# Kernel optimization log

Hardware: AMD Instinct MI355X
Metric: run time of the kernel (lower is better)

Reference implementation:

```python
import jax, jax.numpy as jnp
import numpy as np

PAD = float(-2**32 + 1)


def setup_inputs() -> dict:
    key = jax.random.key(0)
    ks = jax.random.split(key, 10)
    B, S, D = 8, 1024, 1024
    s = 0.02  # keep projections in sane range
    return {
        "Q": jax.random.normal(ks[0], (B, S, D), jnp.float32),
        "K": jax.random.normal(ks[1], (B, S, D), jnp.float32),
        "V": jax.random.normal(ks[2], (B, S, D), jnp.float32),
        "WQ": jax.random.normal(ks[3], (D, D), jnp.float32) * s,
        "bQ": jnp.zeros((D,), jnp.float32),
        "WK": jax.random.normal(ks[4], (D, D), jnp.float32) * s,
        "bK": jnp.zeros((D,), jnp.float32),
        "WV": jax.random.normal(ks[5], (D, D), jnp.float32) * s,
        "bV": jnp.zeros((D,), jnp.float32),
        "WO": jax.random.normal(ks[6], (D, D), jnp.float32) * s,
        "bO": jnp.zeros((D,), jnp.float32),
        "h": 16,
    }


def reference(Q, K, V, WQ, bQ, WK, bK, WV, bV, WO, bO, h):
    B, S, D = Q.shape
    dk = D // h
    # Dense projections with relu activation (as in the Keras layer)
    Qp = jax.nn.relu(Q @ WQ + bQ)
    Kp = jax.nn.relu(K @ WK + bK)
    Vp = jax.nn.relu(V @ WV + bV)
    # tf.concat(tf.split(x, h, axis=2), axis=0): head-major stacking -> (h, B, S, dk)
    qh = Qp.reshape(B, S, h, dk).transpose(2, 0, 1, 3)
    kh = Kp.reshape(B, S, h, dk).transpose(2, 0, 1, 3)
    vh = Vp.reshape(B, S, h, dk).transpose(2, 0, 1, 3)
    # scaled dot product; NOTE: source scales by 1/sqrt(d_model), not 1/sqrt(d_k)
    scores = jnp.einsum('hbqd,hbkd->hbqk', qh, kh) / jnp.sqrt(jnp.float32(D))
    # key padding mask: zero key rows -> large negative
    kmask = jnp.sum(jnp.abs(kh), axis=-1) != 0  # (h,B,Tk)
    scores = jnp.where(kmask[:, :, None, :], scores, PAD)
    w = jax.nn.softmax(scores, axis=-1)
    # query padding mask: zero query rows -> zero weights
    qmask = jnp.sign(jnp.sum(jnp.abs(qh), axis=-1))  # (h,B,Tq), 0/1
    w = w * qmask[:, :, :, None]
    # dropout_prob = 0.0 -> identity
    out = jnp.einsum('hbqk,hbkd->hbqd', w, vh)
    # tf.concat(tf.split(dot_product, h, axis=0), axis=2) -> (B,S,h*dk)
    out = out.transpose(1, 2, 0, 3).reshape(B, S, D)
    return jax.nn.relu(out @ WO + bO)
```

## Files before the change

kernel.cpp:

```cpp
#include <hip/hip_runtime.h>
#include <hip/hip_bf16.h>
#include <cstdint>

#define DEV __device__ __forceinline__

typedef __attribute__((ext_vector_type(4))) float f32x4;
typedef __attribute__((ext_vector_type(8))) short b16x8;
typedef __attribute__((ext_vector_type(4))) unsigned short u16x4;
typedef __attribute__((ext_vector_type(8))) unsigned short u16x8;
typedef __attribute__((ext_vector_type(2))) unsigned int u32x2;

typedef __attribute__((address_space(1))) void gvoid_t;
typedef __attribute__((address_space(3))) void lvoid_t;

static constexpr int Bsz = 8, Ssz = 1024, Dsz = 1024;
static constexpr int Mrows = Bsz * Ssz;

DEV void gld16(const void* g, void* l) {
  __builtin_amdgcn_global_load_lds((gvoid_t*)(uintptr_t)g,
                                   (lvoid_t*)(unsigned)(uintptr_t)l, 16, 0, 0);
}

DEV unsigned short f2bf(float x) {
  unsigned int u = __float_as_uint(x);
  u += 0x7fffu + ((u >> 16) & 1u);
  return (unsigned short)(u >> 16);
}

DEV unsigned int cvt2(float lo, float hi) {
  __hip_bfloat162 h = __float22bfloat162_rn(make_float2(lo, hi));
  unsigned int u;
  __builtin_memcpy(&u, &h, 4);
  return u;
}

__global__ __launch_bounds__(256) void wconv_kernel(
    const float* __restrict__ WQ, const float* __restrict__ WK,
    const float* __restrict__ WV, const float* __restrict__ WO,
    unsigned short* __restrict__ Wt) {
  __shared__ float tile[64][65];
  const int w = blockIdx.z;
  const float* W = (w == 0) ? WQ : (w == 1) ? WK : (w == 2) ? WV : WO;
  const int k0 = blockIdx.x * 64, n0 = blockIdx.y * 64;
  const int t = threadIdx.x;
  {
    const int r = t >> 4;
    const int c = (t & 15) * 4;
#pragma unroll
    for (int i = 0; i < 4; ++i) {
      f32x4 v = *(const f32x4*)(W + (size_t)(k0 + i * 16 + r) * Dsz + n0 + c);
      tile[i * 16 + r][c + 0] = v[0];
      tile[i * 16 + r][c + 1] = v[1];
      tile[i * 16 + r][c + 2] = v[2];
      tile[i * 16 + r][c + 3] = v[3];
    }
  }
  __syncthreads();
  {
    const int n = t >> 2;
    const int ks = (t & 3) * 16;
    unsigned short* dst =
        Wt + (size_t)w * Dsz * Dsz + (size_t)(n0 + n) * Dsz + k0 + ks;
#pragma unroll
    for (int j = 0; j < 16; j += 4) {
      u16x4 p;
#pragma unroll
      for (int jj = 0; jj < 4; ++jj) p[jj] = f2bf(tile[ks + j + jj][n]);
      *(u16x4*)(dst + j) = p;
    }
  }
}

template <bool A_FP32, int OUT_MODE>
DEV void gemm_body(const void* __restrict__ A_,
                   const unsigned short* __restrict__ Bt,
                   const float* __restrict__ bias, void* __restrict__ C_,
                   int m0, int n0, float outscale) {
  constexpr int Kd = 1024, Nd = 1024;
  __shared__ unsigned short Asl[128 * 64] __attribute__((aligned(16)));
  __shared__ unsigned short Bsl[128 * 64] __attribute__((aligned(16)));
  const int t = threadIdx.x, lane = t & 63, wave = t >> 6;
  const int grp = lane >> 4, r16 = lane & 15;
  const int wm = wave >> 1, wn = wave & 1;
  const int swz = (r16 & 7) << 4;
  f32x4 acc[4][4] = {};
  for (int kt = 0; kt < Kd; kt += 64) {
#pragma unroll
    for (int j = 0; j < 4; ++j) {
      int chunk = (wave * 4 + j) * 64 + lane;
      int row = chunk >> 3, c = chunk & 7;
      int csw = c ^ (row & 7);
      gld16(Bt + (size_t)(n0 + row) * Kd + kt + csw * 8,
            (char*)Bsl + (wave * 4 + j) * 1024);
      if constexpr (!A_FP32) {
        gld16((const unsigned short*)A_ + (size_t)(m0 + row) * Kd + kt + csw * 8,
              (char*)Asl + (wave * 4 + j) * 1024);
      }
    }
    if constexpr (A_FP32) {
      const float* A = (const float*)A_;
#pragma unroll
      for (int it = 0; it < 4; ++it) {
        int chunk = it * 256 + t;
        int row = chunk >> 3, c = chunk & 7;
        int csw = c ^ (row & 7);
        const float* src = A + (size_t)(m0 + row) * Kd + kt + csw * 8;
        f32x4 v0 = *(const f32x4*)src;
        f32x4 v1 = *(const f32x4*)(src + 4);
        u32x2 w0, w1;
        w0[0] = cvt2(v0[0], v0[1]);
        w0[1] = cvt2(v0[2], v0[3]);
        w1[0] = cvt2(v1[0], v1[1]);
        w1[1] = cvt2(v1[2], v1[3]);
        *(u32x2*)((char*)Asl + chunk * 16) = w0;
        *(u32x2*)((char*)Asl + chunk * 16 + 8) = w1;
      }
    }
    __syncthreads();
#pragma unroll
    for (int cs = 0; cs < 2; ++cs) {
      b16x8 af[4], bfr[4];
#pragma unroll
      for (int mi = 0; mi < 4; ++mi)
        af[mi] = *(const b16x8*)((char*)Asl + (wm * 64 + mi * 16 + r16) * 128 +
                                 ((cs * 64 + grp * 16) ^ swz));
#pragma unroll
      for (int ni = 0; ni < 4; ++ni)
        bfr[ni] = *(const b16x8*)((char*)Bsl + (wn * 64 + ni * 16 + r16) * 128 +
                                  ((cs * 64 + grp * 16) ^ swz));
#pragma unroll
      for (int mi = 0; mi < 4; ++mi)
#pragma unroll
        for (int ni = 0; ni < 4; ++ni)
          acc[mi][ni] = __builtin_amdgcn_mfma_f32_16x16x32_bf16(
              af[mi], bfr[ni], acc[mi][ni], 0, 0, 0);
    }
    __syncthreads();
  }
#pragma unroll
  for (int mi = 0; mi < 4; ++mi) {
#pragma unroll
    for (int ni = 0; ni < 4; ++ni) {
      int col = n0 + wn * 64 + ni * 16 + r16;
      float bv = bias[col];
      int row0 = m0 + wm * 64 + mi * 16 + grp * 4;
      if constexpr (OUT_MODE == 2) {
        int bb = row0 >> 10, s = row0 & 1023;
        u16x4 pk;
#pragma unroll
        for (int r = 0; r < 4; ++r)
          pk[r] = f2bf(fmaxf(acc[mi][ni][r] + bv, 0.0f) * outscale);
        *(u16x4*)((unsigned short*)C_ +
                  (((size_t)(bb * 1024 + col)) << 10) + s) = pk;
      } else {
#pragma unroll
        for (int r = 0; r < 4; ++r) {
          float v = fmaxf(acc[mi][ni][r] + bv, 0.0f) * outscale;
          if constexpr (OUT_MODE == 1)
            ((unsigned short*)C_)[(size_t)(row0 + r) * Nd + col] = f2bf(v);
          else
            ((float*)C_)[(size_t)(row0 + r) * Nd + col] = v;
        }
      }
    }
  }
}

static constexpr float QSCALE = 0.03125f * 1.4426950408889634f;

__global__ __launch_bounds__(256) void proj3_kernel(
    const float* __restrict__ Q, const float* __restrict__ K,
    const float* __restrict__ V, const unsigned short* __restrict__ Wt,
    const float* __restrict__ bQ, const float* __restrict__ bK,
    const float* __restrict__ bV, unsigned short* __restrict__ Qp,
    unsigned short* __restrict__ Kp, unsigned short* __restrict__ VpT) {
  const size_t DD = (size_t)Dsz * Dsz;
  const int bid = blockIdx.x;
  const int id2 = (bid & 7) * 64 + (bid >> 3);
  const int n0 = (id2 & 7) * 128, m0 = (id2 >> 3) * 128;
  const int z = blockIdx.z;
  if (z == 0)
    gemm_body<true, 1>(Q, Wt, bQ, Qp, m0, n0, QSCALE);
  else if (z == 1)
    gemm_body<true, 1>(K, Wt + DD, bK, Kp, m0, n0, 1.0f);
  else
    gemm_body<true, 2>(V, Wt + 2 * DD, bV, VpT, m0, n0, 1.0f);
}

__global__ __launch_bounds__(256) void out_gemm_kernel(
    const unsigned short* __restrict__ AO,
    const unsigned short* __restrict__ WOt, const float* __restrict__ bO,
    float* __restrict__ Out) {
  const int bid = blockIdx.x;
  const int id2 = (bid & 7) * 64 + (bid >> 3);
  const int n0 = (id2 & 7) * 128, m0 = (id2 >> 3) * 128;
  gemm_body<false, 0>(AO, WOt, bO, Out, m0, n0, 1.0f);
}

__global__ __launch_bounds__(512, 4) void attn_kernel(
    const unsigned short* __restrict__ Qp, const unsigned short* __restrict__ Kp,
    const unsigned short* __restrict__ VpT, unsigned short* __restrict__ AO) {
  __shared__ unsigned short Ks[2][64 * 64] __attribute__((aligned(16)));
  __shared__ unsigned short Vs[2][64 * 64] __attribute__((aligned(16)));
  __shared__ unsigned short Ps[16][16 * 64] __attribute__((aligned(16)));
  const int t = threadIdx.x, lane = t & 63, wave = t >> 6;
  const int grp = lane >> 4, r16 = lane & 15;
  const int bid = blockIdx.x;
  const int id2 = (bid & 7) * 64 + (bid >> 3);
  const int q0 = (id2 & 3) * 256;
  const int bh = id2 >> 2;
  const int b = bh & 7, head = bh >> 3;

  const int srow = t >> 3, scc = t & 7;
  const int csw = scc ^ (srow & 7);
  const unsigned short* kbase = Kp + ((size_t)b * Ssz) * Dsz + head * 64;
  const unsigned short* vbase = VpT + ((size_t)b * Dsz + head * 64) * Ssz;

  const int sqA = q0 + wave * 16 + r16;
  const unsigned short* qbA = Qp + ((size_t)b * Ssz + sqA) * Dsz + head * 64;
  const unsigned short* qbB = qbA + (size_t)128 * Dsz;
  b16x8 qfA0 = *(const b16x8*)(qbA + grp * 8);
  b16x8 qfA1 = *(const b16x8*)(qbA + 32 + grp * 8);
  b16x8 qfB0 = *(const b16x8*)(qbB + grp * 8);
  b16x8 qfB1 = *(const b16x8*)(qbB + 32 + grp * 8);

  f32x4 oA[4] = {}, oB[4] = {};
  f32x4 olA = {}, olB = {};
  const f32x4 zero4 = {0.0f, 0.0f, 0.0f, 0.0f};
  const b16x8 ones = {16256, 16256, 16256, 16256,
                      16256, 16256, 16256, 16256};

  auto stage = [&](int kv0, int pb) {
    gld16(kbase + (size_t)(kv0 + srow) * Dsz + csw * 8,
          (char*)Ks[pb] + wave * 1024);
    gld16(vbase + (size_t)srow * Ssz + kv0 + csw * 8,
          (char*)Vs[pb] + wave * 1024);
  };

  stage(0, 0);
  __syncthreads();
  int cur = 0;

  for (int it = 0; it < 16; ++it) {
    if (it < 15) stage((it + 1) * 64, cur ^ 1);

    __builtin_amdgcn_s_setprio(1);
    f32x4 scA[4], scB[4];
#pragma unroll
    for (int f = 0; f < 4; ++f) {
      int k = f * 16 + r16;
      int kswz = (k & 7) << 4;
      const char* kb = (const char*)Ks[cur] + k * 128;
      b16x8 kf0 = *(const b16x8*)(kb + ((grp * 16) ^ kswz));
      b16x8 kf1 = *(const b16x8*)(kb + ((64 + grp * 16) ^ kswz));
      f32x4 sA = __builtin_amdgcn_mfma_f32_16x16x32_bf16(kf0, qfA0, zero4, 0, 0, 0);
      scA[f] = __builtin_amdgcn_mfma_f32_16x16x32_bf16(kf1, qfA1, sA, 0, 0, 0);
      f32x4 sB = __builtin_amdgcn_mfma_f32_16x16x32_bf16(kf0, qfB0, zero4, 0, 0, 0);
      scB[f] = __builtin_amdgcn_mfma_f32_16x16x32_bf16(kf1, qfB1, sB, 0, 0, 0);
    }
    __builtin_amdgcn_s_setprio(0);

    {
      int qs = (r16 & 7) << 4;
      char* prowA = (char*)Ps + (wave * 2 + 0) * 2048 + r16 * 128;
      char* prowB = (char*)Ps + (wave * 2 + 1) * 2048 + r16 * 128;
#pragma unroll
      for (int f = 0; f < 4; ++f) {
        u32x2 w;
        w[0] = cvt2(exp2f(scA[f][0]), exp2f(scA[f][1]));
        w[1] = cvt2(exp2f(scA[f][2]), exp2f(scA[f][3]));
        *(u32x2*)(prowA + ((f * 32 + grp * 8) ^ qs)) = w;
      }
#pragma unroll
      for (int f = 0; f < 4; ++f) {
        u32x2 w;
        w[0] = cvt2(exp2f(scB[f][0]), exp2f(scB[f][1]));
        w[1] = cvt2(exp2f(scB[f][2]), exp2f(scB[f][3]));
        *(u32x2*)(prowB + ((f * 32 + grp * 8) ^ qs)) = w;
      }
    }

    __builtin_amdgcn_s_setprio(1);
#pragma unroll
    for (int ks = 0; ks < 2; ++ks) {
      int pswz = (r16 & 7) << 4;
      int poff = r16 * 128 + ((ks * 64 + grp * 16) ^ pswz);
      b16x8 paA = *(const b16x8*)((char*)Ps + (wave * 2 + 0) * 2048 + poff);
      b16x8 paB = *(const b16x8*)((char*)Ps + (wave * 2 + 1) * 2048 + poff);
      olA = __builtin_amdgcn_mfma_f32_16x16x32_bf16(paA, ones, olA, 0, 0, 0);
      olB = __builtin_amdgcn_mfma_f32_16x16x32_bf16(paB, ones, olB, 0, 0, 0);
#pragma unroll
      for (int fc = 0; fc < 4; ++fc) {
        int d = fc * 16 + r16;
        int vswz = (d & 7) << 4;
        b16x8 vb = *(const b16x8*)((char*)Vs[cur] + d * 128 +
                                   ((ks * 64 + grp * 16) ^ vswz));
        oA[fc] = __builtin_amdgcn_mfma_f32_16x16x32_bf16(paA, vb, oA[fc], 0, 0, 0);
        oB[fc] = __builtin_amdgcn_mfma_f32_16x16x32_bf16(paB, vb, oB[fc], 0, 0, 0);
      }
    }
    __builtin_amdgcn_s_setprio(0);
    __syncthreads();
    cur ^= 1;
  }

#pragma unroll
  for (int fc = 0; fc < 4; ++fc) {
    int col = head * 64 + fc * 16 + r16;
#pragma unroll
    for (int r = 0; r < 4; ++r) {
      int rowA = q0 + wave * 16 + grp * 4 + r;
      AO[((size_t)b * Ssz + rowA) * Dsz + col] = f2bf(oA[fc][r] / olA[r]);
      AO[((size_t)b * Ssz + rowA + 128) * Dsz + col] = f2bf(oB[fc][r] / olB[r]);
    }
  }
}

extern "C" void kernel_launch(void* const* d_in, const int* in_sizes, int n_in,
                              void* d_out, int out_size, void* d_ws,
                              size_t ws_size, hipStream_t stream) {
  const float* Q = (const float*)d_in[0];
  const float* K = (const float*)d_in[1];
  const float* V = (const float*)d_in[2];
  const float* WQ = (const float*)d_in[3];
  const float* bQ = (const float*)d_in[4];
  const float* WK = (const float*)d_in[5];
  const float* bK = (const float*)d_in[6];
  const float* WV = (const float*)d_in[7];
  const float* bV = (const float*)d_in[8];
  const float* WO = (const float*)d_in[9];
  const float* bO = (const float*)d_in[10];

  char* ws = (char*)d_ws;
  const size_t MB = 1024ull * 1024ull;
  const size_t DD = (size_t)Dsz * Dsz;
  unsigned short* Wt = (unsigned short*)(ws);
  unsigned short* Qp = (unsigned short*)(ws + 8 * MB);
  unsigned short* Kp = (unsigned short*)(ws + 24 * MB);
  unsigned short* VpT = (unsigned short*)(ws + 40 * MB);
  unsigned short* AO = (unsigned short*)(ws + 56 * MB);

  wconv_kernel<<<dim3(16, 16, 4), 256, 0, stream>>>(WQ, WK, WV, WO, Wt);
  proj3_kernel<<<dim3(512, 1, 3), 256, 0, stream>>>(Q, K, V, Wt, bQ, bK, bV,
                                                    Qp, Kp, VpT);
  attn_kernel<<<512, 512, 0, stream>>>(Qp, Kp, VpT, AO);
  out_gemm_kernel<<<512, 256, 0, stream>>>(AO, Wt + 3 * DD, bO, (float*)d_out);
}
```

Measured before the change: 174.0 us.

## Pre-convert Q/K/V activations to bf16 and split projection GEMMs

Adds standalone fp32-to-bf16 conversion kernels for Q, K and V, so the projection GEMMs can load A tiles with async global_load_lds like the output GEMM. Inside the GEMM loop, the register-staged fp32 loads and in-loop conversion are removed. The fused three-way projection is split into a Q/K launch and a separate V launch, reusing workspace buffers. This adds extra full passes over the activations in HBM plus two more kernel launches.

```diff
diff --git a/kernel.cpp b/kernel.cpp
--- a/kernel.cpp
+++ b/kernel.cpp
@@ -71,8 +71,32 @@
   }
 }
 
-template <bool A_FP32, int OUT_MODE>
-DEV void gemm_body(const void* __restrict__ A_,
+DEV void conv_body(const float* __restrict__ src,
+                   unsigned short* __restrict__ dst, int bid) {
+  size_t i = ((size_t)bid * 256 + threadIdx.x) * 8;
+  f32x4 a = *(const f32x4*)(src + i);
+  f32x4 b = *(const f32x4*)(src + i + 4);
+  u16x8 p;
+  p[0] = f2bf(a[0]); p[1] = f2bf(a[1]); p[2] = f2bf(a[2]); p[3] = f2bf(a[3]);
+  p[4] = f2bf(b[0]); p[5] = f2bf(b[1]); p[6] = f2bf(b[2]); p[7] = f2bf(b[3]);
+  *(u16x8*)(dst + i) = p;
+}
+
+__global__ __launch_bounds__(256) void conv2_kernel(
+    const float* __restrict__ s0, unsigned short* __restrict__ d0,
+    const float* __restrict__ s1, unsigned short* __restrict__ d1) {
+  const int bid = blockIdx.x;
+  if (bid < 4096) conv_body(s0, d0, bid);
+  else conv_body(s1, d1, bid - 4096);
+}
+
+__global__ __launch_bounds__(256) void conv_kernel(
+    const float* __restrict__ src, unsigned short* __restrict__ dst) {
+  conv_body(src, dst, blockIdx.x);
+}
+
+template <int OUT_MODE>
+DEV void gemm_body(const unsigned short* __restrict__ A,
                    const unsigned short* __restrict__ Bt,
                    const float* __restrict__ bias, void* __restrict__ C_,
                    int m0, int n0, float outscale) {
@@ -92,29 +116,8 @@
       int csw = c ^ (row & 7);
       gld16(Bt + (size_t)(n0 + row) * Kd + kt + csw * 8,
             (char*)Bsl + (wave * 4 + j) * 1024);
-      if constexpr (!A_FP32) {
-        gld16((const unsigned short*)A_ + (size_t)(m0 + row) * Kd + kt + csw * 8,
-              (char*)Asl + (wave * 4 + j) * 1024);
-      }
-    }
-    if constexpr (A_FP32) {
-      const float* A = (const float*)A_;
-#pragma unroll
-      for (int it = 0; it < 4; ++it) {
-        int chunk = it * 256 + t;
-        int row = chunk >> 3, c = chunk & 7;
-        int csw = c ^ (row & 7);
-        const float* src = A + (size_t)(m0 + row) * Kd + kt + csw * 8;
-        f32x4 v0 = *(const f32x4*)src;
-        f32x4 v1 = *(const f32x4*)(src + 4);
-        u32x2 w0, w1;
-        w0[0] = cvt2(v0[0], v0[1]);
-        w0[1] = cvt2(v0[2], v0[3]);
-        w1[0] = cvt2(v1[0], v1[1]);
-        w1[1] = cvt2(v1[2], v1[3]);
-        *(u32x2*)((char*)Asl + chunk * 16) = w0;
-        *(u32x2*)((char*)Asl + chunk * 16 + 8) = w1;
-      }
+      gld16(A + (size_t)(m0 + row) * Kd + kt + csw * 8,
+            (char*)Asl + (wave * 4 + j) * 1024);
     }
     __syncthreads();
 #pragma unroll
@@ -168,23 +171,30 @@
 
 static constexpr float QSCALE = 0.03125f * 1.4426950408889634f;
 
-__global__ __launch_bounds__(256) void proj3_kernel(
-    const float* __restrict__ Q, const float* __restrict__ K,
-    const float* __restrict__ V, const unsigned short* __restrict__ Wt,
-    const float* __restrict__ bQ, const float* __restrict__ bK,
-    const float* __restrict__ bV, unsigned short* __restrict__ Qp,
-    unsigned short* __restrict__ Kp, unsigned short* __restrict__ VpT) {
+__global__ __launch_bounds__(256) void projqk_kernel(
+    const unsigned short* __restrict__ Qc, const unsigned short* __restrict__ Kc,
+    const unsigned short* __restrict__ Wt, const float* __restrict__ bQ,
+    const float* __restrict__ bK, unsigned short* __restrict__ Qp,
+    unsigned short* __restrict__ Kp) {
   const size_t DD = (size_t)Dsz * Dsz;
+  const int bid = blockIdx.x;
+  const int id2 = (bid & 7) * 128 + (bid >> 3);
+  const int z = id2 >> 9;
+  const int rem = id2 & 511;
+  const int n0 = (rem & 7) * 128, m0 = (rem >> 3) * 128;
+  if (z == 0)
+    gemm_body<1>(Qc, Wt, bQ, Qp, m0, n0, QSCALE);
+  else
+    gemm_body<1>(Kc, Wt + DD, bK, Kp, m0, n0, 1.0f);
+}
+
+__global__ __launch_bounds__(256) void projv_kernel(
+    const unsigned short* __restrict__ Vc, const unsigned short* __restrict__ Wt,
+    const float* __restrict__ bV, unsigned short* __restrict__ VpT) {
   const int bid = blockIdx.x;
   const int id2 = (bid & 7) * 64 + (bid >> 3);
   const int n0 = (id2 & 7) * 128, m0 = (id2 >> 3) * 128;
-  const int z = blockIdx.z;
-  if (z == 0)
-    gemm_body<true, 1>(Q, Wt, bQ, Qp, m0, n0, QSCALE);
-  else if (z == 1)
-    gemm_body<true, 1>(K, Wt + DD, bK, Kp, m0, n0, 1.0f);
-  else
-    gemm_body<true, 2>(V, Wt + 2 * DD, bV, VpT, m0, n0, 1.0f);
+  gemm_body<2>(Vc, Wt + 2 * (size_t)Dsz * Dsz, bV, VpT, m0, n0, 1.0f);
 }
 
 __global__ __launch_bounds__(256) void out_gemm_kernel(
@@ -194,7 +204,7 @@
   const int bid = blockIdx.x;
   const int id2 = (bid & 7) * 64 + (bid >> 3);
   const int n0 = (id2 & 7) * 128, m0 = (id2 >> 3) * 128;
-  gemm_body<false, 0>(AO, WOt, bO, Out, m0, n0, 1.0f);
+  gemm_body<0>(AO, WOt, bO, Out, m0, n0, 1.0f);
 }
 
 __global__ __launch_bounds__(512, 4) void attn_kernel(
@@ -335,14 +345,16 @@
   const size_t MB = 1024ull * 1024ull;
   const size_t DD = (size_t)Dsz * Dsz;
   unsigned short* Wt = (unsigned short*)(ws);
-  unsigned short* Qp = (unsigned short*)(ws + 8 * MB);
-  unsigned short* Kp = (unsigned short*)(ws + 24 * MB);
-  unsigned short* VpT = (unsigned short*)(ws + 40 * MB);
-  unsigned short* AO = (unsigned short*)(ws + 56 * MB);
+  unsigned short* R1 = (unsigned short*)(ws + 8 * MB);
+  unsigned short* R2 = (unsigned short*)(ws + 24 * MB);
+  unsigned short* R3 = (unsigned short*)(ws + 40 * MB);
+  unsigned short* R4 = (unsigned short*)(ws + 56 * MB);
 
   wconv_kernel<<<dim3(16, 16, 4), 256, 0, stream>>>(WQ, WK, WV, WO, Wt);
-  proj3_kernel<<<dim3(512, 1, 3), 256, 0, stream>>>(Q, K, V, Wt, bQ, bK, bV,
-                                                    Qp, Kp, VpT);
-  attn_kernel<<<512, 512, 0, stream>>>(Qp, Kp, VpT, AO);
-  out_gemm_kernel<<<512, 256, 0, stream>>>(AO, Wt + 3 * DD, bO, (float*)d_out);
-}
+  conv2_kernel<<<8192, 256, 0, stream>>>(Q, R4, K, R3);
+  projqk_kernel<<<1024, 256, 0, stream>>>(R4, R3, Wt, bQ, bK, R1, R2);
+  conv_kernel<<<4096, 256, 0, stream>>>(V, R4);
+  projv_kernel<<<512, 256, 0, stream>>>(R4, Wt, bV, R3);
+  attn_kernel<<<512, 512, 0, stream>>>(R1, R2, R3, R4);
+  out_gemm_kernel<<<512, 256, 0, stream>>>(R4, Wt + 3 * DD, bO, (float*)d_out);
+}
```

Result: slower. 185.2 us (+6.5%).
